# Optimization experiments

Hardware: AMD Instinct MI355X
Metric: run time of the kernel (lower is better)

Reference implementation:

```python
import jax, jax.numpy as jnp
import numpy as np

B, S, D = 2, 2048, 2048
H, HK, HD = 16, 4, 128          # query heads, kv heads, head dim (H*HD == D)
HID = 4 * D                      # SwiGLU hidden (mult=4)
WIN, SINK = 1024, 4              # sliding window, attention sink tokens
EPS = 1e-6
ROPE_BASE = 10000.0


def rmsnorm(x, g):
    return x * jax.lax.rsqrt(jnp.mean(x * x, axis=-1, keepdims=True) + EPS) * g


def rope_tables(seq_len, head_dim):
    inv = 1.0 / (ROPE_BASE ** (jnp.arange(0, head_dim, 2, dtype=jnp.float32) / head_dim))
    ang = jnp.arange(seq_len, dtype=jnp.float32)[:, None] * inv[None, :]  # [S, HD/2]
    return jnp.cos(ang), jnp.sin(ang)


def apply_rope(x, cos, sin):
    # x: [B, S, h, HD]; rotate-half convention
    x1, x2 = jnp.split(x, 2, axis=-1)
    c = cos[None, :, None, :]
    s = sin[None, :, None, :]
    return jnp.concatenate([x1 * c - x2 * s, x2 * c + x1 * s], axis=-1)


def setup_inputs() -> dict:
    key = jax.random.key(0)
    ks = jax.random.split(key, 10)
    p = 0.02
    return {
        "x": jax.random.normal(ks[0], (B, S, D), dtype=jnp.float32),
        "g1": jnp.ones((D,), dtype=jnp.float32),
        "g2": jnp.ones((D,), dtype=jnp.float32),
        "wq": jax.random.normal(ks[1], (D, H * HD), dtype=jnp.float32) * p,
        "wk": jax.random.normal(ks[2], (D, HK * HD), dtype=jnp.float32) * p,
        "wv": jax.random.normal(ks[3], (D, HK * HD), dtype=jnp.float32) * p,
        "wo": jax.random.normal(ks[4], (H * HD, D), dtype=jnp.float32) * p,
        "w_gate": jax.random.normal(ks[5], (D, HID), dtype=jnp.float32) * p,
        "w_up": jax.random.normal(ks[6], (D, HID), dtype=jnp.float32) * p,
        "w_down": jax.random.normal(ks[7], (HID, D), dtype=jnp.float32) * p,
    }


def reference(x, g1, g2, wq, wk, wv, wo, w_gate, w_up, w_down):
    # ---- pre-norm attention ----
    h = rmsnorm(x, g1)
    q = (h @ wq).reshape(B, S, H, HD)
    k = (h @ wk).reshape(B, S, HK, HD)
    v = (h @ wv).reshape(B, S, HK, HD)

    cos, sin = rope_tables(S, HD)
    q = apply_rope(q, cos, sin)
    k = apply_rope(k, cos, sin)

    # GQA: expand kv heads to query heads
    rep = H // HK
    k = jnp.repeat(k, rep, axis=2)  # [B, S, H, HD]
    v = jnp.repeat(v, rep, axis=2)

    scores = jnp.einsum("bqhd,bkhd->bhqk", q, k) / jnp.sqrt(jnp.float32(HD))

    # causal + sliding-window + attention-sink mask
    i = jnp.arange(S)[:, None]
    j = jnp.arange(S)[None, :]
    allowed = (j <= i) & (((i - j) < WIN) | (j < SINK))  # [S, S]
    scores = jnp.where(allowed[None, None], scores, jnp.float32(-1e9))

    attn = jax.nn.softmax(scores, axis=-1)
    a = jnp.einsum("bhqk,bkhd->bqhd", attn, v).reshape(B, S, H * HD) @ wo

    x = x + a

    # ---- pre-norm SwiGLU FFN ----
    h2 = rmsnorm(x, g2)
    ffn = (jax.nn.silu(h2 @ w_gate) * (h2 @ w_up)) @ w_down
    return x + ffn
```

## Files before the change

### kernel.cpp

```cpp
#include <hip/hip_runtime.h>
#include <hip/hip_bf16.h>
#include <stdint.h>

#define TOK 4096
#define SEQ 2048
#define DM 2048
#define NH 16
#define NKV 4
#define HDIM 128
#define HID 8192
#define WIN 1024
#define SINKN 4

typedef float f32x4 __attribute__((ext_vector_type(4)));
typedef __bf16 bf16x8 __attribute__((ext_vector_type(8)));
typedef unsigned short u16;
typedef unsigned int u32;

#define VM(n) asm volatile("s_waitcnt vmcnt(" #n ")" ::: "memory")

__device__ __forceinline__ u16 f2bf(float f) {
  union { float f; u32 u; } v; v.f = f;
  return (u16)((v.u + 0x7fffu + ((v.u >> 16) & 1u)) >> 16);
}
__device__ __forceinline__ float bf2f(u16 h) {
  union { u32 u; float f; } v; v.u = ((u32)h) << 16;
  return v.f;
}
__device__ __forceinline__ f32x4 mfma16(bf16x8 a, bf16x8 b, f32x4 c) {
  return __builtin_amdgcn_mfma_f32_16x16x32_bf16(a, b, c, 0, 0, 0);
}
__device__ __forceinline__ void gld16(const u16* g, u16* l) {
  __builtin_amdgcn_global_load_lds(
      (const __attribute__((address_space(1))) u32*)g,
      (__attribute__((address_space(3))) u32*)l, 16, 0, 0);
}
__device__ __forceinline__ void bar() {
  asm volatile("s_barrier" ::: "memory");
}
__device__ __forceinline__ void swz_rc(int c, int& row, int& k8) {
  row = 2 * (c >> 3) + (((c >> 2) & 1) ^ ((c >> 4) & 1));
  k8 = (c & 3) ^ (row & 3);
}
__device__ __forceinline__ void raster8(int wg, int nwg, int nbx, int& bx, int& by) {
  int cpx = nwg >> 3;
  int s = (wg & 7) * cpx + (wg >> 3);
  by = 8 * (s / (8 * nbx)) + (s & 7);
  bx = (s >> 3) % nbx;
}

__global__ __launch_bounds__(256)
void wtrans(const float* __restrict__ in, u16* __restrict__ out, int K, int N)
{
  __shared__ float t[32][33];
  int tx = threadIdx.x & 31, ty = threadIdx.x >> 5;
  int bx = blockIdx.x, by = blockIdx.y;
  #pragma unroll
  for (int i = 0; i < 4; i++) {
    int r = ty + i * 8;
    t[r][tx] = in[(size_t)(by * 32 + r) * N + bx * 32 + tx];
  }
  __syncthreads();
  #pragma unroll
  for (int i = 0; i < 4; i++) {
    int r = ty + i * 8;
    out[(size_t)(bx * 32 + r) * K + by * 32 + tx] = f2bf(t[tx][r]);
  }
}

__global__ __launch_bounds__(256)
void vtrans(const u16* __restrict__ in, int ld, u16* __restrict__ out)
{
  __shared__ u16 t[32][33];
  int tx = threadIdx.x & 31, ty = threadIdx.x >> 5;
  int bx = blockIdx.x;
  int by = blockIdx.y;
  #pragma unroll
  for (int i = 0; i < 4; i++) {
    int r = ty + i * 8;
    t[r][tx] = in[(size_t)(by * 32 + r) * ld + bx * 32 + tx];
  }
  __syncthreads();
  int b = (by * 32) >> 11;
  int s0 = (by * 32) & (SEQ - 1);
  #pragma unroll
  for (int i = 0; i < 4; i++) {
    int c = bx * 32 + ty + i * 8;
    out[(size_t)(b * (NKV * HDIM) + c) * SEQ + s0 + tx] = t[tx][ty + i * 8];
  }
}

__global__ __launch_bounds__(256)
void rope_table_k(float* __restrict__ ct, float* __restrict__ st)
{
  int idx = blockIdx.x * 256 + threadIdx.x;
  int pos = idx >> 6, d = idx & 63;
  float inv = powf(10000.0f, -(float)d / 64.0f);
  float a = (float)pos * inv;
  ct[idx] = cosf(a);
  st[idx] = sinf(a);
}

__global__ void rope_apply_k(u16* __restrict__ q, int ld,
                             const float* __restrict__ ct,
                             const float* __restrict__ st, float scale)
{
  int t = blockIdx.x;
  int hh = threadIdx.x >> 6;
  int d = threadIdx.x & 63;
  int pos = t & (SEQ - 1);
  size_t base = (size_t)t * ld + hh * HDIM + d;
  float x1 = bf2f(q[base]), x2 = bf2f(q[base + 64]);
  float c = ct[pos * 64 + d], s = st[pos * 64 + d];
  q[base]      = f2bf((x1 * c - x2 * s) * scale);
  q[base + 64] = f2bf((x2 * c + x1 * s) * scale);
}

__global__ __launch_bounds__(256)
void rmsnorm_k(const float* __restrict__ x, const float* __restrict__ g,
               u16* __restrict__ o)
{
  int row = blockIdx.x;
  int tid = threadIdx.x;
  const float* xr = x + (size_t)row * DM;
  float4 v0 = *(const float4*)(xr + tid * 8);
  float4 v1 = *(const float4*)(xr + tid * 8 + 4);
  float ss = v0.x*v0.x + v0.y*v0.y + v0.z*v0.z + v0.w*v0.w
           + v1.x*v1.x + v1.y*v1.y + v1.z*v1.z + v1.w*v1.w;
  #pragma unroll
  for (int d = 1; d < 64; d <<= 1) ss += __shfl_xor(ss, d);
  __shared__ float red[4];
  if ((tid & 63) == 0) red[tid >> 6] = ss;
  __syncthreads();
  float inv = rsqrtf((red[0] + red[1] + red[2] + red[3]) * (1.0f / DM) + 1e-6f);
  float4 g0 = *(const float4*)(g + tid * 8);
  float4 g1 = *(const float4*)(g + tid * 8 + 4);
  ushort4 o0, o1;
  o0.x = f2bf(v0.x * inv * g0.x); o0.y = f2bf(v0.y * inv * g0.y);
  o0.z = f2bf(v0.z * inv * g0.z); o0.w = f2bf(v0.w * inv * g0.w);
  o1.x = f2bf(v1.x * inv * g1.x); o1.y = f2bf(v1.y * inv * g1.y);
  o1.z = f2bf(v1.z * inv * g1.z); o1.w = f2bf(v1.w * inv * g1.w);
  *(ushort4*)(o + (size_t)row * DM + tid * 8) = o0;
  *(ushort4*)(o + (size_t)row * DM + tid * 8 + 4) = o1;
}

template<int BM, int EPI>
__global__ __launch_bounds__(512, 2)
void gemm8(const u16* __restrict__ A, const u16* __restrict__ Bt,
           u16* __restrict__ Cb, float* __restrict__ Cf,
           const float* __restrict__ X, int M, int N, int K, int nbx)
{
  constexpr int BN = 256;
  constexpr int MREP = BM / 32;
  constexpr int ASZ = BM * 32;
  constexpr int SLOT = ASZ + BN * 32;
  __shared__ u16 lds[4 * SLOT];

  int bx, by;
  raster8(blockIdx.x, gridDim.x, nbx, bx, by);
  int m0 = by * BM, n0 = bx * BN;

  int tid = threadIdx.x;
  int l = tid & 63, w = tid >> 6;
  int l16 = l & 15, lg = l >> 4;
  int wr = w >> 2, wc = w & 3;

  int aoff[MREP], boff[4];
  #pragma unroll
  for (int m = 0; m < MREP; m++) {
    int ar = wr * (BM / 2) + m * 16 + l16;
    aoff[m] = (ar * 32 + lg * 8) ^ ((ar & 7) * 8);
  }
  #pragma unroll
  for (int n = 0; n < 4; n++) {
    int br = wc * 64 + n * 16 + l16;
    boff[n] = ASZ + ((br * 32 + lg * 8) ^ ((br & 7) * 8));
  }

  const u16 *srcA0, *srcA1, *srcB0, *srcB1;
  {
    int r, kc;
    swz_rc(tid, r, kc);
    srcA0 = A + (size_t)(m0 + r) * K + kc * 8;
    srcB0 = Bt + (size_t)(n0 + r) * K + kc * 8;
    swz_rc(tid + 512, r, kc);
    srcB1 = Bt + (size_t)(n0 + r) * K + kc * 8;
    srcA1 = (BM == 256) ? (A + (size_t)(m0 + r) * K + kc * 8) : srcA0;
  }

  const int NT = K >> 5;

  auto stageA = [&](int t) {
    u16* d = lds + (t & 3) * SLOT;
    gld16(srcA0 + t * 32, d + tid * 8);
    if constexpr (BM == 256) gld16(srcA1 + t * 32, d + (tid + 512) * 8);
  };
  auto stageB = [&](int t) {
    u16* d = lds + (t & 3) * SLOT + ASZ;
    gld16(srcB0 + t * 32, d + tid * 8);
    gld16(srcB1 + t * 32, d + (tid + 512) * 8);
  };

  stageA(0); stageB(0); stageA(1); stageB(1); stageA(2); stageB(2);
  if constexpr (BM == 256) VM(8); else VM(6);
  bar();

  f32x4 acc[MREP][4];
  f32x4 zero = {0.f, 0.f, 0.f, 0.f};
  #pragma unroll
  for (int m = 0; m < MREP; m++)
    #pragma unroll
    for (int n = 0; n < 4; n++) acc[m][n] = zero;

  for (int j = 0; j < NT; ++j) {
    u16* cur = lds + (j & 3) * SLOT;
    const bool st = (j + 3 < NT);

    if (st) stageA(j + 3);
    bf16x8 a[MREP], b0, b1;
    #pragma unroll
    for (int mf = 0; mf < MREP; mf++) a[mf] = *(const bf16x8*)(cur + aoff[mf]);
    b0 = *(const bf16x8*)(cur + boff[0]);
    b1 = *(const bf16x8*)(cur + boff[1]);
    bar();
    asm volatile("s_waitcnt lgkmcnt(0)" ::: "memory");
    __builtin_amdgcn_sched_barrier(0);
    __builtin_amdgcn_s_setprio(1);
    #pragma unroll
    for (int mf = 0; mf < MREP; mf++) {
      acc[mf][0] = mfma16(a[mf], b0, acc[mf][0]);
      acc[mf][1] = mfma16(a[mf], b1, acc[mf][1]);
    }
    __builtin_amdgcn_s_setprio(0);
    __builtin_amdgcn_sched_barrier(0);
    bar();

    if (st) stageB(j + 3);
    b0 = *(const bf16x8*)(cur + boff[2]);
    b1 = *(const bf16x8*)(cur + boff[3]);
    if constexpr (BM == 256) {
      if (st) VM(8); else if (j + 2 < NT) VM(4); else VM(0);
    } else {
      if (st) VM(6); else if (j + 2 < NT) VM(3); else VM(0);
    }
    bar();
    asm volatile("s_waitcnt lgkmcnt(0)" ::: "memory");
    __builtin_amdgcn_sched_barrier(0);
    __builtin_amdgcn_s_setprio(1);
    #pragma unroll
    for (int mf = 0; mf < MREP; mf++) {
      acc[mf][2] = mfma16(a[mf], b0, acc[mf][2]);
      acc[mf][3] = mfma16(a[mf], b1, acc[mf][3]);
    }
    __builtin_amdgcn_s_setprio(0);
    __builtin_amdgcn_sched_barrier(0);
    bar();
  }

  #pragma unroll
  for (int m = 0; m < MREP; m++) {
    int row = m0 + wr * (BM / 2) + m * 16 + lg * 4;
    #pragma unroll
    for (int n = 0; n < 4; n++) {
      int col = n0 + wc * 64 + n * 16 + l16;
      #pragma unroll
      for (int r = 0; r < 4; r++) {
        size_t idx = (size_t)(row + r) * N + col;
        float v = acc[m][n][r];
        if (EPI == 0) {
          Cb[idx] = f2bf(v);
        } else if (EPI == 1) {
          Cf[idx] = X[idx] + v;
        } else {
          Cf[idx] += v;
        }
      }
    }
  }
}

__global__ __launch_bounds__(512, 2)
void gemm8gu(const u16* __restrict__ A, const u16* __restrict__ Bg,
             const u16* __restrict__ Bu, u16* __restrict__ Gu, int K, int nbx)
{
  constexpr int BM = 256;
  constexpr int MREP = 8;
  constexpr int ASZ = BM * 32;
  constexpr int SLOT = ASZ + 256 * 32;
  __shared__ u16 lds[4 * SLOT];

  int bx, by;
  raster8(blockIdx.x, gridDim.x, nbx, bx, by);
  int m0 = by * BM, n0 = bx * 128;

  int tid = threadIdx.x;
  int l = tid & 63, w = tid >> 6;
  int l16 = l & 15, lg = l >> 4;
  int wr = w >> 2, wc = w & 3;

  int aoff[MREP], boff[4];
  #pragma unroll
  for (int m = 0; m < MREP; m++) {
    int ar = wr * 128 + m * 16 + l16;
    aoff[m] = (ar * 32 + lg * 8) ^ ((ar & 7) * 8);
  }
  #pragma unroll
  for (int n = 0; n < 4; n++) {
    int br = (n >> 1) * 128 + wc * 32 + (n & 1) * 16 + l16;
    boff[n] = ASZ + ((br * 32 + lg * 8) ^ ((br & 7) * 8));
  }

  const u16 *srcA0, *srcA1, *srcB0, *srcB1;
  {
    int r, kc;
    swz_rc(tid, r, kc);
    srcA0 = A + (size_t)(m0 + r) * K + kc * 8;
    srcB0 = ((r < 128) ? Bg + (size_t)(n0 + r) * K
                       : Bu + (size_t)(n0 + r - 128) * K) + kc * 8;
    swz_rc(tid + 512, r, kc);
    srcA1 = A + (size_t)(m0 + r) * K + kc * 8;
    srcB1 = ((r < 128) ? Bg + (size_t)(n0 + r) * K
                       : Bu + (size_t)(n0 + r - 128) * K) + kc * 8;
  }

  const int NT = K >> 5;

  auto stageA = [&](int t) {
    u16* d = lds + (t & 3) * SLOT;
    gld16(srcA0 + t * 32, d + tid * 8);
    gld16(srcA1 + t * 32, d + (tid + 512) * 8);
  };
  auto stageB = [&](int t) {
    u16* d = lds + (t & 3) * SLOT + ASZ;
    gld16(srcB0 + t * 32, d + tid * 8);
    gld16(srcB1 + t * 32, d + (tid + 512) * 8);
  };

  stageA(0); stageB(0); stageA(1); stageB(1); stageA(2); stageB(2);
  VM(8);
  bar();

  f32x4 acc[MREP][4];
  f32x4 zero = {0.f, 0.f, 0.f, 0.f};
  #pragma unroll
  for (int m = 0; m < MREP; m++)
    #pragma unroll
    for (int n = 0; n < 4; n++) acc[m][n] = zero;

  for (int j = 0; j < NT; ++j) {
    u16* cur = lds + (j & 3) * SLOT;
    const bool st = (j + 3 < NT);

    if (st) stageA(j + 3);
    bf16x8 a[MREP], b0, b1;
    #pragma unroll
    for (int mf = 0; mf < MREP; mf++) a[mf] = *(const bf16x8*)(cur + aoff[mf]);
    b0 = *(const bf16x8*)(cur + boff[0]);
    b1 = *(const bf16x8*)(cur + boff[1]);
    bar();
    asm volatile("s_waitcnt lgkmcnt(0)" ::: "memory");
    __builtin_amdgcn_sched_barrier(0);
    __builtin_amdgcn_s_setprio(1);
    #pragma unroll
    for (int mf = 0; mf < MREP; mf++) {
      acc[mf][0] = mfma16(a[mf], b0, acc[mf][0]);
      acc[mf][1] = mfma16(a[mf], b1, acc[mf][1]);
    }
    __builtin_amdgcn_s_setprio(0);
    __builtin_amdgcn_sched_barrier(0);
    bar();

    if (st) stageB(j + 3);
    b0 = *(const bf16x8*)(cur + boff[2]);
    b1 = *(const bf16x8*)(cur + boff[3]);
    if (st) VM(8); else if (j + 2 < NT) VM(4); else VM(0);
    bar();
    asm volatile("s_waitcnt lgkmcnt(0)" ::: "memory");
    __builtin_amdgcn_sched_barrier(0);
    __builtin_amdgcn_s_setprio(1);
    #pragma unroll
    for (int mf = 0; mf < MREP; mf++) {
      acc[mf][2] = mfma16(a[mf], b0, acc[mf][2]);
      acc[mf][3] = mfma16(a[mf], b1, acc[mf][3]);
    }
    __builtin_amdgcn_s_setprio(0);
    __builtin_amdgcn_sched_barrier(0);
    bar();
  }

  #pragma unroll
  for (int m = 0; m < MREP; m++) {
    int row = m0 + wr * 128 + m * 16 + lg * 4;
    #pragma unroll
    for (int n = 0; n < 2; n++) {
      int col = n0 + wc * 32 + n * 16 + l16;
      #pragma unroll
      for (int r = 0; r < 4; r++) {
        float gt = acc[m][n][r];
        float up = acc[m][n + 2][r];
        float sg = gt / (1.0f + __expf(-gt));
        Gu[(size_t)(row + r) * HID + col] = f2bf(sg * up);
      }
    }
  }
}

__global__ __launch_bounds__(256)
void attn_k(const u16* __restrict__ qb, int ldq,
            const u16* __restrict__ kb, int ldk,
            const u16* __restrict__ vbt, u16* __restrict__ ao)
{
  int q0 = blockIdx.x * 128;
  int h = blockIdx.y;
  int b = blockIdx.z;
  int hk = h >> 2;
  int tid = threadIdx.x;
  int w = tid >> 6, l = tid & 63;
  int l16 = l & 15, lg = l >> 4;

  __shared__ u16 Ks[32 * 128];
  __shared__ u16 Vt[128 * 32];
  __shared__ u16 Ps[4][32 * 40];
  u16* Pw = Ps[w];

  bf16x8 qf[2][4];
  #pragma unroll
  for (int m = 0; m < 2; m++)
    #pragma unroll
    for (int kd = 0; kd < 4; kd++) {
      int row = q0 + w * 32 + m * 16 + l16;
      qf[m][kd] = *(const bf16x8*)(qb + (size_t)(b * SEQ + row) * ldq
                                   + h * HDIM + kd * 32 + lg * 8);
    }

  f32x4 oacc[2][8];
  float mrun[2][4], lrun[2][4];
  f32x4 zero = {0.f, 0.f, 0.f, 0.f};
  #pragma unroll
  for (int m = 0; m < 2; m++) {
    #pragma unroll
    for (int nd = 0; nd < 8; nd++) oacc[m][nd] = zero;
    #pragma unroll
    for (int r = 0; r < 4; r++) { mrun[m][r] = -1e9f; lrun[m][r] = 0.f; }
  }

  int kr0 = tid >> 4,        kc0 = (tid & 15) ^ (kr0 & 7);
  int kr1 = (tid + 256) >> 4, kc1 = (tid & 15) ^ (kr1 & 7);
  int vd0, vk0, vd1, vk1;
  swz_rc(tid, vd0, vk0);
  swz_rc(tid + 256, vd1, vk1);
  const u16* kbase = kb + (size_t)(b * SEQ) * ldk + hk * HDIM;
  const u16* vbase = vbt + (size_t)(b * NKV + hk) * HDIM * SEQ;

  int koff[2][4];
  #pragma unroll
  for (int n = 0; n < 2; n++)
    #pragma unroll
    for (int kd = 0; kd < 4; kd++) {
      int key = n * 16 + l16;
      koff[n][kd] = ((key * 128) + kd * 32 + lg * 8) ^ ((key & 7) * 8);
    }
  int voff[8];
  #pragma unroll
  for (int nd = 0; nd < 8; nd++) {
    int d = nd * 16 + l16;
    voff[nd] = (d * 32 + lg * 8) ^ ((d & 7) * 8);
  }

  int lo = (q0 >= WIN) ? ((q0 - (WIN - 1)) >> 5) : 0;
  int hi = (q0 + 127) >> 5;

  for (int it = (lo > 0 ? lo - 1 : 0); it <= hi; ++it) {
    int kt = (it < lo) ? 0 : it;
    gld16(kbase + (size_t)(kt * 32 + kr0) * ldk + kc0 * 8, Ks + tid * 8);
    gld16(kbase + (size_t)(kt * 32 + kr1) * ldk + kc1 * 8, Ks + (tid + 256) * 8);
    gld16(vbase + (size_t)vd0 * SEQ + kt * 32 + vk0 * 8, Vt + tid * 8);
    gld16(vbase + (size_t)vd1 * SEQ + kt * 32 + vk1 * 8, Vt + (tid + 256) * 8);
    __syncthreads();

    f32x4 sacc[2][2];
    sacc[0][0] = zero; sacc[0][1] = zero; sacc[1][0] = zero; sacc[1][1] = zero;
    #pragma unroll
    for (int kd = 0; kd < 4; kd++) {
      bf16x8 kf0 = *(const bf16x8*)(Ks + koff[0][kd]);
      bf16x8 kf1 = *(const bf16x8*)(Ks + koff[1][kd]);
      #pragma unroll
      for (int m = 0; m < 2; m++) {
        sacc[m][0] = mfma16(qf[m][kd], kf0, sacc[m][0]);
        sacc[m][1] = mfma16(qf[m][kd], kf1, sacc[m][1]);
      }
    }

    #pragma unroll
    for (int m = 0; m < 2; m++) {
      float sc[4];
      #pragma unroll
      for (int r = 0; r < 4; r++) {
        int i = q0 + w * 32 + m * 16 + lg * 4 + r;
        int j0 = kt * 32 + l16;
        int j1 = j0 + 16;
        float s0 = sacc[m][0][r];
        float s1 = sacc[m][1][r];
        bool ok0 = (j0 <= i) && ((i - j0 < WIN) || (j0 < SINKN));
        bool ok1 = (j1 <= i) && ((i - j1 < WIN) || (j1 < SINKN));
        s0 = ok0 ? s0 : -1e9f;
        s1 = ok1 ? s1 : -1e9f;
        float mx = fmaxf(s0, s1);
        mx = fmaxf(mx, __shfl_xor(mx, 1));
        mx = fmaxf(mx, __shfl_xor(mx, 2));
        mx = fmaxf(mx, __shfl_xor(mx, 4));
        mx = fmaxf(mx, __shfl_xor(mx, 8));
        float mold = mrun[m][r];
        float mnew = fmaxf(mold, mx);
        float scl = __expf(mold - mnew);
        mrun[m][r] = mnew;
        float p0 = __expf(s0 - mnew);
        float p1 = __expf(s1 - mnew);
        int prow = m * 16 + lg * 4 + r;
        Pw[prow * 40 + l16] = f2bf(p0);
        Pw[prow * 40 + 16 + l16] = f2bf(p1);
        float ps = p0 + p1;
        ps += __shfl_xor(ps, 1);
        ps += __shfl_xor(ps, 2);
        ps += __shfl_xor(ps, 4);
        ps += __shfl_xor(ps, 8);
        lrun[m][r] = lrun[m][r] * scl + ps;
        sc[r] = scl;
      }
      #pragma unroll
      for (int nd = 0; nd < 8; nd++) {
        oacc[m][nd][0] *= sc[0];
        oacc[m][nd][1] *= sc[1];
        oacc[m][nd][2] *= sc[2];
        oacc[m][nd][3] *= sc[3];
      }
    }

    bf16x8 pa0 = *(const bf16x8*)(Pw + l16 * 40 + lg * 8);
    bf16x8 pa1 = *(const bf16x8*)(Pw + (16 + l16) * 40 + lg * 8);
    #pragma unroll
    for (int nd = 0; nd < 8; nd++) {
      bf16x8 vf = *(const bf16x8*)(Vt + voff[nd]);
      oacc[0][nd] = mfma16(pa0, vf, oacc[0][nd]);
      oacc[1][nd] = mfma16(pa1, vf, oacc[1][nd]);
    }
    __syncthreads();
  }

  #pragma unroll
  for (int m = 0; m < 2; m++)
    #pragma unroll
    for (int r = 0; r < 4; r++) {
      float invl = 1.0f / lrun[m][r];
      int row = q0 + w * 32 + m * 16 + lg * 4 + r;
      #pragma unroll
      for (int nd = 0; nd < 8; nd++) {
        int col = nd * 16 + l16;
        ao[(size_t)(b * SEQ + row) * (NH * HDIM) + h * HDIM + col] =
            f2bf(oacc[m][nd][r] * invl);
      }
    }
}

extern "C" void kernel_launch(void* const* d_in, const int* in_sizes, int n_in,
                              void* d_out, int out_size, void* d_ws, size_t ws_size,
                              hipStream_t stream)
{
  (void)in_sizes; (void)n_in; (void)out_size;
  const float* x  = (const float*)d_in[0];
  const float* g1 = (const float*)d_in[1];
  const float* g2 = (const float*)d_in[2];
  const float* wq = (const float*)d_in[3];
  const float* wk = (const float*)d_in[4];
  const float* wv = (const float*)d_in[5];
  const float* wo = (const float*)d_in[6];
  const float* wg = (const float*)d_in[7];
  const float* wu = (const float*)d_in[8];
  const float* wd = (const float*)d_in[9];
  float* out = (float*)d_out;

  char* ws = (char*)d_ws;
  size_t off = 0;
  auto alloc = [&](size_t bytes) {
    char* p = ws + off;
    off += (bytes + 255) & ~(size_t)255;
    return p;
  };
  const int NQKV = 3072;
  u16* wqkv_t = (u16*)alloc((size_t)NQKV * DM * 2);
  u16* wo_t   = (u16*)alloc((size_t)DM * DM * 2);
  u16* wg_t   = (u16*)alloc((size_t)HID * DM * 2);
  u16* wu_t   = (u16*)alloc((size_t)HID * DM * 2);
  u16* wd_t   = (u16*)alloc((size_t)DM * HID * 2);
  u16* hb     = (u16*)alloc((size_t)TOK * DM * 2);
  char* span0 = ws + off;
  u16* qkvb   = (u16*)alloc((size_t)TOK * NQKV * 2);
  u16* vbt    = (u16*)alloc((size_t)TOK * NKV * HDIM * 2);
  u16* aob    = (u16*)alloc((size_t)TOK * NH * HDIM * 2);
  size_t span_used = (size_t)(ws + off - span0);
  size_t gu_need = (size_t)TOK * HID * 2;
  if (gu_need > span_used) alloc(gu_need - span_used);
  u16* gu = (u16*)span0;
  float* ct  = (float*)alloc((size_t)SEQ * 64 * 4);
  float* st  = (float*)alloc((size_t)SEQ * 64 * 4);
  if (off > ws_size) return;

  dim3 blk(256);
  dim3 blk512(512);

  wtrans<<<dim3(DM / 32, DM / 32), blk, 0, stream>>>(wq, wqkv_t, DM, DM);
  wtrans<<<dim3((NKV * HDIM) / 32, DM / 32), blk, 0, stream>>>(wk, wqkv_t + (size_t)DM * DM, DM, NKV * HDIM);
  wtrans<<<dim3((NKV * HDIM) / 32, DM / 32), blk, 0, stream>>>(wv, wqkv_t + (size_t)(DM + NKV * HDIM) * DM, DM, NKV * HDIM);
  wtrans<<<dim3(DM / 32, DM / 32), blk, 0, stream>>>(wo, wo_t, DM, DM);
  wtrans<<<dim3(HID / 32, DM / 32), blk, 0, stream>>>(wg, wg_t, DM, HID);
  wtrans<<<dim3(HID / 32, DM / 32), blk, 0, stream>>>(wu, wu_t, DM, HID);
  wtrans<<<dim3(DM / 32, HID / 32), blk, 0, stream>>>(wd, wd_t, HID, DM);

  rope_table_k<<<SEQ * 64 / 256, blk, 0, stream>>>(ct, st);
  rmsnorm_k<<<TOK, blk, 0, stream>>>(x, g1, hb);

  gemm8<128, 0><<<dim3((NQKV / 256) * (TOK / 128)), blk512, 0, stream>>>(
      hb, wqkv_t, qkvb, nullptr, nullptr, TOK, NQKV, DM, NQKV / 256);

  rope_apply_k<<<TOK, dim3(NH * 64), 0, stream>>>(qkvb, NQKV, ct, st, 0.08838834764831845f);
  rope_apply_k<<<TOK, dim3(NKV * 64), 0, stream>>>(qkvb + DM, NQKV, ct, st, 1.0f);
  vtrans<<<dim3((NKV * HDIM) / 32, TOK / 32), blk, 0, stream>>>(qkvb + DM + NKV * HDIM, NQKV, vbt);

  attn_k<<<dim3(SEQ / 128, NH, 2), blk, 0, stream>>>(qkvb, NQKV, qkvb + DM, NQKV, vbt, aob);

  gemm8<128, 1><<<dim3((DM / 256) * (TOK / 128)), blk512, 0, stream>>>(
      aob, wo_t, nullptr, out, x, TOK, DM, DM, DM / 256);
  rmsnorm_k<<<TOK, blk, 0, stream>>>(out, g2, hb);

  gemm8gu<<<dim3((HID / 128) * (TOK / 256)), blk512, 0, stream>>>(
      hb, wg_t, wu_t, gu, DM, HID / 128);

  gemm8<128, 3><<<dim3((DM / 256) * (TOK / 128)), blk512, 0, stream>>>(
      gu, wd_t, nullptr, out, nullptr, TOK, DM, HID, DM / 256);
}
```

Measured before the change: 848.1 us.

## Unify GEMMs into one kernel with K=64 tiles and triple-buffered LDS

Replaces the separate gemm8 and gemm8gu kernels with a single templated gemmp kernel. It uses 128-row tiles with a K-step of 64, three LDS buffers instead of four, a new XOR swizzle, and launch bounds of one block per CU. The gate/up GEMM now uses 128x128 output tiles instead of 256-row ones. The aim is to halve the number of loop iterations and barriers per K and to do more MFMA work per barrier. The cost is less occupancy, a shallower prefetch depth, and less A-tile reuse in the gate/up GEMM.

```diff
diff --git a/kernel.cpp b/kernel.cpp
--- a/kernel.cpp
+++ b/kernel.cpp
@@ -18,6 +18,7 @@
 typedef unsigned int u32;
 
 #define VM(n) asm volatile("s_waitcnt vmcnt(" #n ")" ::: "memory")
+#define LGKM0 asm volatile("s_waitcnt lgkmcnt(0)" ::: "memory")
 
 __device__ __forceinline__ u16 f2bf(float f) {
   union { float f; u32 u; } v; v.f = f;
@@ -144,262 +145,173 @@
   *(ushort4*)(o + (size_t)row * DM + tid * 8 + 4) = o1;
 }
 
-template<int BM, int EPI>
-__global__ __launch_bounds__(512, 2)
-void gemm8(const u16* __restrict__ A, const u16* __restrict__ Bt,
-           u16* __restrict__ Cb, float* __restrict__ Cf,
-           const float* __restrict__ X, int M, int N, int K, int nbx)
-{
-  constexpr int BN = 256;
-  constexpr int MREP = BM / 32;
-  constexpr int ASZ = BM * 32;
-  constexpr int SLOT = ASZ + BN * 32;
-  __shared__ u16 lds[4 * SLOT];
+template<int EPI, int GU>
+__global__ __launch_bounds__(512, 1)
+void gemmp(const u16* __restrict__ A, const u16* __restrict__ Bt,
+           const u16* __restrict__ Bu, u16* __restrict__ Cb,
+           float* __restrict__ Cf, const float* __restrict__ X,
+           int M, int N, int K, int nbx)
+{
+  constexpr int ASZ = 128 * 64;
+  constexpr int SLOT = ASZ + 256 * 64;
+  __shared__ u16 lds[3 * SLOT];
 
   int bx, by;
   raster8(blockIdx.x, gridDim.x, nbx, bx, by);
-  int m0 = by * BM, n0 = bx * BN;
+  int m0 = by * 128;
+  int n0 = bx * (GU ? 128 : 256);
 
   int tid = threadIdx.x;
   int l = tid & 63, w = tid >> 6;
   int l16 = l & 15, lg = l >> 4;
   int wr = w >> 2, wc = w & 3;
 
-  int aoff[MREP], boff[4];
-  #pragma unroll
-  for (int m = 0; m < MREP; m++) {
-    int ar = wr * (BM / 2) + m * 16 + l16;
-    aoff[m] = (ar * 32 + lg * 8) ^ ((ar & 7) * 8);
-  }
-  #pragma unroll
-  for (int n = 0; n < 4; n++) {
-    int br = wc * 64 + n * 16 + l16;
-    boff[n] = ASZ + ((br * 32 + lg * 8) ^ ((br & 7) * 8));
-  }
-
-  const u16 *srcA0, *srcA1, *srcB0, *srcB1;
-  {
-    int r, kc;
-    swz_rc(tid, r, kc);
-    srcA0 = A + (size_t)(m0 + r) * K + kc * 8;
-    srcB0 = Bt + (size_t)(n0 + r) * K + kc * 8;
-    swz_rc(tid + 512, r, kc);
-    srcB1 = Bt + (size_t)(n0 + r) * K + kc * 8;
-    srcA1 = (BM == 256) ? (A + (size_t)(m0 + r) * K + kc * 8) : srcA0;
-  }
-
-  const int NT = K >> 5;
-
-  auto stageA = [&](int t) {
-    u16* d = lds + (t & 3) * SLOT;
-    gld16(srcA0 + t * 32, d + tid * 8);
-    if constexpr (BM == 256) gld16(srcA1 + t * 32, d + (tid + 512) * 8);
+  int aoff[4][2], boff[4][2];
+  #pragma unroll
+  for (int m = 0; m < 4; m++)
+    #pragma unroll
+    for (int kk = 0; kk < 2; kk++) {
+      int row = wr * 64 + m * 16 + l16;
+      aoff[m][kk] = ((row * 128 + kk * 64 + lg * 16) ^ ((row & 7) << 4)) >> 1;
+    }
+  #pragma unroll
+  for (int n = 0; n < 4; n++)
+    #pragma unroll
+    for (int kk = 0; kk < 2; kk++) {
+      int br = GU ? ((n >> 1) * 128 + wc * 32 + (n & 1) * 16 + l16)
+                  : (wc * 64 + n * 16 + l16);
+      boff[n][kk] = ASZ + (((br * 128 + kk * 64 + lg * 16) ^ ((br & 7) << 4)) >> 1);
+    }
+
+  int urow = tid >> 3;
+  int cc = (tid & 7) ^ (urow & 7);
+  const u16* pA[2];
+  const u16* pB[4];
+  pA[0] = A + (size_t)(m0 + urow) * K + cc * 8;
+  pA[1] = A + (size_t)(m0 + 64 + urow) * K + cc * 8;
+  #pragma unroll
+  for (int u = 0; u < 4; u++) {
+    if (GU) pB[u] = (u < 2 ? Bt + (size_t)(n0 + u * 64 + urow) * K
+                           : Bu + (size_t)(n0 + (u - 2) * 64 + urow) * K) + cc * 8;
+    else    pB[u] = Bt + (size_t)(n0 + u * 64 + urow) * K + cc * 8;
+  }
+
+  const int NT = K >> 6;
+
+  auto stA = [&](int tt, int u) {
+    gld16(pA[u] + (size_t)tt * 64, lds + (tt % 3) * SLOT + u * 4096 + tid * 8);
   };
-  auto stageB = [&](int t) {
-    u16* d = lds + (t & 3) * SLOT + ASZ;
-    gld16(srcB0 + t * 32, d + tid * 8);
-    gld16(srcB1 + t * 32, d + (tid + 512) * 8);
+  auto stB = [&](int tt, int u) {
+    gld16(pB[u] + (size_t)tt * 64, lds + (tt % 3) * SLOT + ASZ + u * 4096 + tid * 8);
   };
 
-  stageA(0); stageB(0); stageA(1); stageB(1); stageA(2); stageB(2);
-  if constexpr (BM == 256) VM(8); else VM(6);
+  #pragma unroll
+  for (int u = 0; u < 4; u++) stB(0, u);
+  stA(0, 0); stA(0, 1);
+  #pragma unroll
+  for (int u = 0; u < 4; u++) stB(1, u);
+  stA(1, 0); stA(1, 1);
+  VM(6);
   bar();
 
-  f32x4 acc[MREP][4];
+  f32x4 acc[4][4];
   f32x4 zero = {0.f, 0.f, 0.f, 0.f};
   #pragma unroll
-  for (int m = 0; m < MREP; m++)
+  for (int m = 0; m < 4; m++)
     #pragma unroll
     for (int n = 0; n < 4; n++) acc[m][n] = zero;
 
-  for (int j = 0; j < NT; ++j) {
-    u16* cur = lds + (j & 3) * SLOT;
-    const bool st = (j + 3 < NT);
-
-    if (st) stageA(j + 3);
-    bf16x8 a[MREP], b0, b1;
-    #pragma unroll
-    for (int mf = 0; mf < MREP; mf++) a[mf] = *(const bf16x8*)(cur + aoff[mf]);
-    b0 = *(const bf16x8*)(cur + boff[0]);
-    b1 = *(const bf16x8*)(cur + boff[1]);
+  for (int t = 0; t < NT; ++t) {
+    u16* cur = lds + (t % 3) * SLOT;
+    const bool st = (t + 2 < NT);
+
+    if (st) { stB(t + 2, 0); stB(t + 2, 1); stB(t + 2, 2); }
+    bf16x8 a[4][2], b[2][2];
+    #pragma unroll
+    for (int m = 0; m < 4; m++) {
+      a[m][0] = *(const bf16x8*)(cur + aoff[m][0]);
+      a[m][1] = *(const bf16x8*)(cur + aoff[m][1]);
+    }
+    #pragma unroll
+    for (int n = 0; n < 2; n++) {
+      b[n][0] = *(const bf16x8*)(cur + boff[n][0]);
+      b[n][1] = *(const bf16x8*)(cur + boff[n][1]);
+    }
     bar();
-    asm volatile("s_waitcnt lgkmcnt(0)" ::: "memory");
+    LGKM0;
     __builtin_amdgcn_sched_barrier(0);
     __builtin_amdgcn_s_setprio(1);
     #pragma unroll
-    for (int mf = 0; mf < MREP; mf++) {
-      acc[mf][0] = mfma16(a[mf], b0, acc[mf][0]);
-      acc[mf][1] = mfma16(a[mf], b1, acc[mf][1]);
-    }
+    for (int m = 0; m < 4; m++)
+      #pragma unroll
+      for (int n = 0; n < 2; n++) {
+        acc[m][n] = mfma16(a[m][0], b[n][0], acc[m][n]);
+        acc[m][n] = mfma16(a[m][1], b[n][1], acc[m][n]);
+      }
     __builtin_amdgcn_s_setprio(0);
     __builtin_amdgcn_sched_barrier(0);
     bar();
 
-    if (st) stageB(j + 3);
-    b0 = *(const bf16x8*)(cur + boff[2]);
-    b1 = *(const bf16x8*)(cur + boff[3]);
-    if constexpr (BM == 256) {
-      if (st) VM(8); else if (j + 2 < NT) VM(4); else VM(0);
-    } else {
-      if (st) VM(6); else if (j + 2 < NT) VM(3); else VM(0);
-    }
+    if (st) { stB(t + 2, 3); stA(t + 2, 0); stA(t + 2, 1); }
+    bf16x8 c2[2][2];
+    #pragma unroll
+    for (int n = 0; n < 2; n++) {
+      c2[n][0] = *(const bf16x8*)(cur + boff[n + 2][0]);
+      c2[n][1] = *(const bf16x8*)(cur + boff[n + 2][1]);
+    }
+    if (st) { VM(6); }
+    else if (t + 1 < NT) { VM(0); }
     bar();
-    asm volatile("s_waitcnt lgkmcnt(0)" ::: "memory");
+    LGKM0;
     __builtin_amdgcn_sched_barrier(0);
     __builtin_amdgcn_s_setprio(1);
     #pragma unroll
-    for (int mf = 0; mf < MREP; mf++) {
-      acc[mf][2] = mfma16(a[mf], b0, acc[mf][2]);
-      acc[mf][3] = mfma16(a[mf], b1, acc[mf][3]);
-    }
+    for (int m = 0; m < 4; m++)
+      #pragma unroll
+      for (int n = 0; n < 2; n++) {
+        acc[m][n + 2] = mfma16(a[m][0], c2[n][0], acc[m][n + 2]);
+        acc[m][n + 2] = mfma16(a[m][1], c2[n][1], acc[m][n + 2]);
+      }
     __builtin_amdgcn_s_setprio(0);
     __builtin_amdgcn_sched_barrier(0);
     bar();
   }
 
-  #pragma unroll
-  for (int m = 0; m < MREP; m++) {
-    int row = m0 + wr * (BM / 2) + m * 16 + lg * 4;
-    #pragma unroll
-    for (int n = 0; n < 4; n++) {
-      int col = n0 + wc * 64 + n * 16 + l16;
-      #pragma unroll
-      for (int r = 0; r < 4; r++) {
-        size_t idx = (size_t)(row + r) * N + col;
-        float v = acc[m][n][r];
-        if (EPI == 0) {
-          Cb[idx] = f2bf(v);
-        } else if (EPI == 1) {
-          Cf[idx] = X[idx] + v;
-        } else {
-          Cf[idx] += v;
+  if (GU) {
+    #pragma unroll
+    for (int m = 0; m < 4; m++) {
+      int row = m0 + wr * 64 + m * 16 + lg * 4;
+      #pragma unroll
+      for (int n = 0; n < 2; n++) {
+        int col = n0 + wc * 32 + n * 16 + l16;
+        #pragma unroll
+        for (int r = 0; r < 4; r++) {
+          float gt = acc[m][n][r];
+          float up = acc[m][n + 2][r];
+          float sg = gt / (1.0f + __expf(-gt));
+          Cb[(size_t)(row + r) * N + col] = f2bf(sg * up);
         }
       }
     }
-  }
-}
-
-__global__ __launch_bounds__(512, 2)
-void gemm8gu(const u16* __restrict__ A, const u16* __restrict__ Bg,
-             const u16* __restrict__ Bu, u16* __restrict__ Gu, int K, int nbx)
-{
-  constexpr int BM = 256;
-  constexpr int MREP = 8;
-  constexpr int ASZ = BM * 32;
-  constexpr int SLOT = ASZ + 256 * 32;
-  __shared__ u16 lds[4 * SLOT];
-
-  int bx, by;
-  raster8(blockIdx.x, gridDim.x, nbx, bx, by);
-  int m0 = by * BM, n0 = bx * 128;
-
-  int tid = threadIdx.x;
-  int l = tid & 63, w = tid >> 6;
-  int l16 = l & 15, lg = l >> 4;
-  int wr = w >> 2, wc = w & 3;
-
-  int aoff[MREP], boff[4];
-  #pragma unroll
-  for (int m = 0; m < MREP; m++) {
-    int ar = wr * 128 + m * 16 + l16;
-    aoff[m] = (ar * 32 + lg * 8) ^ ((ar & 7) * 8);
-  }
-  #pragma unroll
-  for (int n = 0; n < 4; n++) {
-    int br = (n >> 1) * 128 + wc * 32 + (n & 1) * 16 + l16;
-    boff[n] = ASZ + ((br * 32 + lg * 8) ^ ((br & 7) * 8));
-  }
-
-  const u16 *srcA0, *srcA1, *srcB0, *srcB1;
-  {
-    int r, kc;
-    swz_rc(tid, r, kc);
-    srcA0 = A + (size_t)(m0 + r) * K + kc * 8;
-    srcB0 = ((r < 128) ? Bg + (size_t)(n0 + r) * K
-                       : Bu + (size_t)(n0 + r - 128) * K) + kc * 8;
-    swz_rc(tid + 512, r, kc);
-    srcA1 = A + (size_t)(m0 + r) * K + kc * 8;
-    srcB1 = ((r < 128) ? Bg + (size_t)(n0 + r) * K
-                       : Bu + (size_t)(n0 + r - 128) * K) + kc * 8;
-  }
-
-  const int NT = K >> 5;
-
-  auto stageA = [&](int t) {
-    u16* d = lds + (t & 3) * SLOT;
-    gld16(srcA0 + t * 32, d + tid * 8);
-    gld16(srcA1 + t * 32, d + (tid + 512) * 8);
-  };
-  auto stageB = [&](int t) {
-    u16* d = lds + (t & 3) * SLOT + ASZ;
-    gld16(srcB0 + t * 32, d + tid * 8);
-    gld16(srcB1 + t * 32, d + (tid + 512) * 8);
-  };
-
-  stageA(0); stageB(0); stageA(1); stageB(1); stageA(2); stageB(2);
-  VM(8);
-  bar();
-
-  f32x4 acc[MREP][4];
-  f32x4 zero = {0.f, 0.f, 0.f, 0.f};
-  #pragma unroll
-  for (int m = 0; m < MREP; m++)
-    #pragma unroll
-    for (int n = 0; n < 4; n++) acc[m][n] = zero;
-
-  for (int j = 0; j < NT; ++j) {
-    u16* cur = lds + (j & 3) * SLOT;
-    const bool st = (j + 3 < NT);
-
-    if (st) stageA(j + 3);
-    bf16x8 a[MREP], b0, b1;
-    #pragma unroll
-    for (int mf = 0; mf < MREP; mf++) a[mf] = *(const bf16x8*)(cur + aoff[mf]);
-    b0 = *(const bf16x8*)(cur + boff[0]);
-    b1 = *(const bf16x8*)(cur + boff[1]);
-    bar();
-    asm volatile("s_waitcnt lgkmcnt(0)" ::: "memory");
-    __builtin_amdgcn_sched_barrier(0);
-    __builtin_amdgcn_s_setprio(1);
-    #pragma unroll
-    for (int mf = 0; mf < MREP; mf++) {
-      acc[mf][0] = mfma16(a[mf], b0, acc[mf][0]);
-      acc[mf][1] = mfma16(a[mf], b1, acc[mf][1]);
-    }
-    __builtin_amdgcn_s_setprio(0);
-    __builtin_amdgcn_sched_barrier(0);
-    bar();
-
-    if (st) stageB(j + 3);
-    b0 = *(const bf16x8*)(cur + boff[2]);
-    b1 = *(const bf16x8*)(cur + boff[3]);
-    if (st) VM(8); else if (j + 2 < NT) VM(4); else VM(0);
-    bar();
-    asm volatile("s_waitcnt lgkmcnt(0)" ::: "memory");
-    __builtin_amdgcn_sched_barrier(0);
-    __builtin_amdgcn_s_setprio(1);
-    #pragma unroll
-    for (int mf = 0; mf < MREP; mf++) {
-      acc[mf][2] = mfma16(a[mf], b0, acc[mf][2]);
-      acc[mf][3] = mfma16(a[mf], b1, acc[mf][3]);
-    }
-    __builtin_amdgcn_s_setprio(0);
-    __builtin_amdgcn_sched_barrier(0);
-    bar();
-  }
-
-  #pragma unroll
-  for (int m = 0; m < MREP; m++) {
-    int row = m0 + wr * 128 + m * 16 + lg * 4;
-    #pragma unroll
-    for (int n = 0; n < 2; n++) {
-      int col = n0 + wc * 32 + n * 16 + l16;
-      #pragma unroll
-      for (int r = 0; r < 4; r++) {
-        float gt = acc[m][n][r];
-        float up = acc[m][n + 2][r];
-        float sg = gt / (1.0f + __expf(-gt));
-        Gu[(size_t)(row + r) * HID + col] = f2bf(sg * up);
+  } else {
+    #pragma unroll
+    for (int m = 0; m < 4; m++) {
+      int row = m0 + wr * 64 + m * 16 + lg * 4;
+      #pragma unroll
+      for (int n = 0; n < 4; n++) {
+        int col = n0 + wc * 64 + n * 16 + l16;
+        #pragma unroll
+        for (int r = 0; r < 4; r++) {
+          size_t idx = (size_t)(row + r) * N + col;
+          float v = acc[m][n][r];
+          if (EPI == 0) {
+            Cb[idx] = f2bf(v);
+          } else if (EPI == 1) {
+            Cf[idx] = X[idx] + v;
+          } else {
+            Cf[idx] += v;
+          }
+        }
       }
     }
   }
@@ -619,8 +531,8 @@
   rope_table_k<<<SEQ * 64 / 256, blk, 0, stream>>>(ct, st);
   rmsnorm_k<<<TOK, blk, 0, stream>>>(x, g1, hb);
 
-  gemm8<128, 0><<<dim3((NQKV / 256) * (TOK / 128)), blk512, 0, stream>>>(
-      hb, wqkv_t, qkvb, nullptr, nullptr, TOK, NQKV, DM, NQKV / 256);
+  gemmp<0, 0><<<dim3((NQKV / 256) * (TOK / 128)), blk512, 0, stream>>>(
+      hb, wqkv_t, nullptr, qkvb, nullptr, nullptr, TOK, NQKV, DM, NQKV / 256);
 
   rope_apply_k<<<TOK, dim3(NH * 64), 0, stream>>>(qkvb, NQKV, ct, st, 0.08838834764831845f);
   rope_apply_k<<<TOK, dim3(NKV * 64), 0, stream>>>(qkvb + DM, NQKV, ct, st, 1.0f);
@@ -628,13 +540,13 @@
 
   attn_k<<<dim3(SEQ / 128, NH, 2), blk, 0, stream>>>(qkvb, NQKV, qkvb + DM, NQKV, vbt, aob);
 
-  gemm8<128, 1><<<dim3((DM / 256) * (TOK / 128)), blk512, 0, stream>>>(
-      aob, wo_t, nullptr, out, x, TOK, DM, DM, DM / 256);
+  gemmp<1, 0><<<dim3((DM / 256) * (TOK / 128)), blk512, 0, stream>>>(
+      aob, wo_t, nullptr, nullptr, out, x, TOK, DM, DM, DM / 256);
   rmsnorm_k<<<TOK, blk, 0, stream>>>(out, g2, hb);
 
-  gemm8gu<<<dim3((HID / 128) * (TOK / 256)), blk512, 0, stream>>>(
-      hb, wg_t, wu_t, gu, DM, HID / 128);
-
-  gemm8<128, 3><<<dim3((DM / 256) * (TOK / 128)), blk512, 0, stream>>>(
-      gu, wd_t, nullptr, out, nullptr, TOK, DM, HID, DM / 256);
-}
+  gemmp<0, 1><<<dim3((HID / 128) * (TOK / 128)), blk512, 0, stream>>>(
+      hb, wg_t, wu_t, gu, nullptr, nullptr, TOK, HID, DM, HID / 128);
+
+  gemmp<3, 0><<<dim3((DM / 256) * (TOK / 128)), blk512, 0, stream>>>(
+      gu, wd_t, nullptr, nullptr, out, nullptr, TOK, DM, HID, DM / 256);
+}
```

After: 821.9 us. 1.03x faster.
